# Optimization experiments

Hardware: AMD Instinct MI355X
Metric: run time of the kernel (lower is better)

Reference implementation:

```python
import jax, jax.numpy as jnp
import numpy as np

EPS = 1e-8


def setup_inputs() -> dict:
    key = jax.random.key(0)
    x = jax.random.normal(key, (16384, 1024), dtype=jnp.float32)
    return {"x": x}


def reference(x) -> jnp.ndarray:
    # L2 normalize along feature dim (torch F.normalize: x / max(||x||, eps))
    norm = jnp.linalg.norm(x, axis=-1, keepdims=True)
    xn = x / jnp.maximum(norm, EPS)

    n = xn.shape[0]
    # full pairwise cosine similarity [N, N]
    dot = xn @ xn.T
    # mask self-similarity on the diagonal
    ii = jnp.arange(n)
    dot = dot.at[ii, ii].set(-1.0)
    # nearest neighbor per row
    index = jnp.argmax(dot, axis=1)

    # torch PairwiseDistance(p=2, eps=1e-8): ||x1 - x2 + eps||_2
    diff = xn - xn[index] + EPS
    distances = jnp.linalg.norm(diff, axis=-1)

    loss = -jnp.mean(jnp.log(distances + EPS))
    return loss
```

## Files before the change

kernel.cpp:

```cpp
#include <hip/hip_runtime.h>
#include <math.h>

#define N 16384
#define D 1024
#define EPSF 1e-8f
#define QSCALE 448.0f
#define NPAIRS 2080
#define NBLK 256
#define PANB 262144
#define BIAS 16777216u

typedef __attribute__((ext_vector_type(4))) int i32x4;
typedef unsigned int u32;
typedef unsigned long long u64;

#define LDS_Bb 65536
#define LDS_TOT 131072

__device__ __forceinline__ void gload_lds16(const void* g, void* l) {
  __builtin_amdgcn_global_load_lds(
      (const __attribute__((address_space(1))) u32*)g,
      (__attribute__((address_space(3))) u32*)l, 16, 0, 0);
}

__device__ __forceinline__ u64 maxu64(u64 x, u64 y) { return x > y ? x : y; }
__device__ __forceinline__ int maxi(int x, int y) { return x > y ? x : y; }

__device__ __forceinline__ void decode_pair(int t, int& a, int& b) {
  int aa = (int)((129.0 - sqrt(129.0 * 129.0 - 8.0 * (double)t)) * 0.5);
  if (aa < 0) aa = 0;
  if (aa > 63) aa = 63;
  while (((aa + 1) * 64 - ((aa + 1) * aa) / 2) <= t) ++aa;
  while ((aa * 64 - (aa * (aa - 1)) / 2) > t) --aa;
  a = aa;
  b = aa + (t - (aa * 64 - (aa * (aa - 1)) / 2));
}


__global__ __launch_bounds__(256) void k_normalize(
    const float* __restrict__ x, signed char* __restrict__ xq,
    float* __restrict__ norms, u64* __restrict__ best) {
  const int w = threadIdx.x >> 6, lane = threadIdx.x & 63;
  const int i = blockIdx.x * 4 + w;
  if (threadIdx.x < 4) best[(size_t)blockIdx.x * 4 + threadIdx.x] = 0;
  const float4* xi = (const float4*)(x + (size_t)i * D);
  float4 v[4];
  float s = 0.f;
#pragma unroll
  for (int t = 0; t < 4; ++t) {
    v[t] = xi[lane + t * 64];
    s += v[t].x * v[t].x + v[t].y * v[t].y + v[t].z * v[t].z + v[t].w * v[t].w;
  }
#pragma unroll
  for (int sh = 32; sh; sh >>= 1) s += __shfl_xor(s, sh, 64);
  const float nrm = sqrtf(s);
  if (lane == 0) norms[i] = nrm;
  const float qs = QSCALE / fmaxf(nrm, EPSF);
  u32* xo = (u32*)(xq + (size_t)i * D);
#pragma unroll
  for (int t = 0; t < 4; ++t) {
    const int q0 = __float2int_rn(fminf(fmaxf(v[t].x * qs, -127.f), 127.f));
    const int q1 = __float2int_rn(fminf(fmaxf(v[t].y * qs, -127.f), 127.f));
    const int q2 = __float2int_rn(fminf(fmaxf(v[t].z * qs, -127.f), 127.f));
    const int q3 = __float2int_rn(fminf(fmaxf(v[t].w * qs, -127.f), 127.f));
    xo[lane + t * 64] = (u32)(q0 & 0xff) | ((u32)(q1 & 0xff) << 8) |
                        ((u32)(q2 & 0xff) << 16) | ((u32)(q3 & 0xff) << 24);
  }
}


#define SGB(gaddr, daddr) \
  gload_lds16(xqB + (gaddr) + srcLane, lds + (daddr) + w * 1024)

#define KT(C_)                                                                 \
  {                                                                            \
    const int k_ = kq * 4 + (C_);                                              \
    const int t_ = k_ + 3;                                                     \
    const int kt_ = t_ & 15;                                                   \
    const size_t aG = (t_ >= 16 ? aPanN : aPan) + (size_t)(kt_ * 64);          \
    const size_t bG = (t_ >= 16 ? bPanN : bPan) + (size_t)(kt_ * 64);          \
    __builtin_amdgcn_s_barrier();                                              \
    asm volatile("" ::: "memory");                                             \
    SGB(aG, (((C_) + 3) & 3) * 16384);                                         \
    SGB(aG + 131072, (((C_) + 3) & 3) * 16384 + 8192);                         \
    SGB(bG, LDS_Bb + (((C_) + 3) & 3) * 16384);                                \
    SGB(bG + 131072, LDS_Bb + (((C_) + 3) & 3) * 16384 + 8192);                \
    i32x4 aa[4], bb[4];                                                        \
    _Pragma("unroll") for (int m = 0; m < 4; ++m) aa[m] =                      \
        *(const i32x4*)(lds + ((C_)&3) * 16384 + aOff[m]);                     \
    _Pragma("unroll") for (int n = 0; n < 4; ++n) bb[n] =                      \
        *(const i32x4*)(lds + LDS_Bb + ((C_)&3) * 16384 + bOff[n]);            \
    __builtin_amdgcn_s_setprio(1);                                             \
    _Pragma("unroll") for (int m = 0; m < 4; ++m)                              \
      _Pragma("unroll") for (int n = 0; n < 4; ++n)                            \
        acc[m][n] = __builtin_amdgcn_mfma_i32_16x16x64_i8(aa[m], bb[n],        \
                                                          acc[m][n], 0, 0, 0); \
    __builtin_amdgcn_s_setprio(0);                                             \
    _Pragma("unroll") for (int n = 0; n < 4; ++n) bb[n] =                      \
        *(const i32x4*)(lds + LDS_Bb + ((C_)&3) * 16384 + bOff[4 + n]);        \
    __builtin_amdgcn_s_setprio(1);                                             \
    _Pragma("unroll") for (int m = 0; m < 4; ++m)                              \
      _Pragma("unroll") for (int n = 0; n < 4; ++n)                            \
        acc[m][4 + n] = __builtin_amdgcn_mfma_i32_16x16x64_i8(                 \
            aa[m], bb[n], acc[m][4 + n], 0, 0, 0);                             \
    __builtin_amdgcn_s_setprio(0);                                             \
    asm volatile("s_waitcnt vmcnt(8)" ::: "memory");                           \
  }

__global__ __launch_bounds__(512, 2) void k_argmax(
    const signed char* __restrict__ xq, u64* __restrict__ best) {
  extern __shared__ char lds[];
  const char* xqB = (const char*)xq;
  const int tid = (int)threadIdx.x, lane = tid & 63, w = tid >> 6;
  const int wr = w >> 1, wc = w & 1;

  int aOff[4], bOff[8];
  const int q = lane >> 4, li = lane & 15;
#pragma unroll
  for (int m = 0; m < 4; ++m) {
    const int rr = wr * 64 + m * 16 + li;
    const int line = rr >> 1;
    aOff[m] = line * 128 + ((((rr & 1) << 6) | (q << 4)) ^ ((line & 7) << 4));
  }
#pragma unroll
  for (int nf = 0; nf < 8; ++nf) {
    const int rr = wc * 128 + nf * 16 + li;
    const int line = rr >> 1;
    bOff[nf] = line * 128 + ((((rr & 1) << 6) | (q << 4)) ^ ((line & 7) << 4));
  }
  const int posx = (lane & 7) ^ (lane >> 3);
  const int rrl = ((w * 8 + (lane >> 3)) << 1) | (posx >> 2);
  const int srcLane = rrl * 1024 + (posx & 3) * 16;

  const int rB2 = wr * 64 + (q << 2);
  const int cB2 = wc * 128 + li;

  const int p0 = ((int)blockIdx.x * NPAIRS) / NBLK;
  const int p1 = (((int)blockIdx.x + 1) * NPAIRS) / NBLK;
  int a, b;
  decode_pair(p0, a, b);
  size_t aPan = (size_t)a * PANB, bPan = (size_t)b * PANB;

  for (int pp = 0; pp < 3; ++pp) {
    SGB(aPan + (size_t)(pp * 64), pp * 16384);
    SGB(aPan + (size_t)(pp * 64) + 131072, pp * 16384 + 8192);
    SGB(bPan + (size_t)(pp * 64), LDS_Bb + pp * 16384);
    SGB(bPan + (size_t)(pp * 64) + 131072, LDS_Bb + pp * 16384 + 8192);
  }
  asm volatile("s_waitcnt vmcnt(8)" ::: "memory");

  i32x4 acc[4][8];
  for (int p = p0; p < p1; ++p) {
    int an = a, bn = b + 1;
    if (bn == 64) {
      an = a + 1;
      bn = an;
    }
    const bool lastp = (p == p1 - 1);
    const size_t aPanN = lastp ? aPan : (size_t)an * PANB;
    const size_t bPanN = lastp ? bPan : (size_t)bn * PANB;

#pragma unroll
    for (int m = 0; m < 4; ++m)
#pragma unroll
      for (int n = 0; n < 8; ++n) acc[m][n] = (i32x4){0, 0, 0, 0};

    for (int kq = 0; kq < 4; ++kq) {
      KT(0)
      KT(1)
      KT(2)
      KT(3)
    }

    const int aBase = a * 256, colBase = b * 256;
#pragma unroll
    for (int m = 0; m < 4; ++m)
#pragma unroll
      for (int r = 0; r < 4; ++r) {
        const int rl = rB2 + m * 16 + r;
        int pk = 0;
        if (a == b) {
#pragma unroll
          for (int nf = 0; nf < 8; ++nf) {
            int v = (int)((((u32)acc[m][nf][r] + BIAS) << 7) |
                          (u32)((nf << 4) | li));
            if (rl == cB2 + nf * 16) v = 0;
            pk = maxi(pk, v);
          }
        } else {
#pragma unroll
          for (int nf = 0; nf < 8; ++nf) {
            const int v = (int)((((u32)acc[m][nf][r] + BIAS) << 7) |
                                (u32)((nf << 4) | li));
            pk = maxi(pk, v);
          }
        }
#pragma unroll
        for (int sh = 1; sh < 16; sh <<= 1) pk = maxi(pk, __shfl_xor(pk, sh, 64));
        if (li == 0) {
          const int dot = (int)((((u32)pk) >> 7) - BIAS);
          const int col = colBase + wc * 128 + (pk & 127);
          const u64 key = ((u64)((u32)dot ^ 0x80000000u) << 32) | (u32)col;
          atomicMax(best + (aBase + rl), key);
        }
      }

    if (a != b) {
#pragma unroll
      for (int nf = 0; nf < 8; ++nf) {
        int pk = 0;
#pragma unroll
        for (int m = 0; m < 4; ++m)
#pragma unroll
          for (int r = 0; r < 4; ++r) {
            const int v = (int)((((u32)acc[m][nf][r] + BIAS) << 6) |
                                (u32)(m * 16 + q * 4 + r));
            pk = maxi(pk, v);
          }
        pk = maxi(pk, __shfl_xor(pk, 16, 64));
        pk = maxi(pk, __shfl_xor(pk, 32, 64));
        if (q == 0) {
          const int dot = (int)((((u32)pk) >> 6) - BIAS);
          const int grow = aBase + wr * 64 + (pk & 63);
          const u64 key = ((u64)((u32)dot ^ 0x80000000u) << 32) | (u32)grow;
          atomicMax(best + (colBase + cB2 + nf * 16), key);
        }
      }
    }

    a = an;
    b = bn;
    aPan = (size_t)a * PANB;
    bPan = (size_t)b * PANB;
  }
}


__global__ __launch_bounds__(256) void k_dist(
    const float* __restrict__ x, const float* __restrict__ norms,
    const u64* __restrict__ best, float* __restrict__ logd) {
  const int w = threadIdx.x >> 6, lane = threadIdx.x & 63;
  const int i = blockIdx.x * 4 + w;
  const u64 p = best[i];
  const int j = (int)(p & 0xffffffffu);
  const float invi = 1.f / fmaxf(norms[i], EPSF);
  const float invj = 1.f / fmaxf(norms[j], EPSF);
  const float4* xi = (const float4*)(x + (size_t)i * D);
  const float4* xj = (const float4*)(x + (size_t)j * D);
  float s = 0.f;
#pragma unroll
  for (int t = 0; t < 4; ++t) {
    const float4 av = xi[lane + t * 64], bv = xj[lane + t * 64];
    float d;
    d = av.x * invi - bv.x * invj + EPSF; s += d * d;
    d = av.y * invi - bv.y * invj + EPSF; s += d * d;
    d = av.z * invi - bv.z * invj + EPSF; s += d * d;
    d = av.w * invi - bv.w * invj + EPSF; s += d * d;
  }
#pragma unroll
  for (int sh = 32; sh; sh >>= 1) s += __shfl_xor(s, sh, 64);
  if (lane == 0) logd[i] = logf(sqrtf(s) + EPSF);
}


__global__ __launch_bounds__(256) void k_final(const float* __restrict__ logd,
                                               float* __restrict__ out) {
  __shared__ double red[256];
  double s = 0.0;
  for (int i = threadIdx.x; i < N; i += 256) s += (double)logd[i];
  red[threadIdx.x] = s;
  __syncthreads();
  for (int sh = 128; sh; sh >>= 1) {
    if ((int)threadIdx.x < sh) red[threadIdx.x] += red[threadIdx.x + sh];
    __syncthreads();
  }
  if (threadIdx.x == 0) out[0] = (float)(-red[0] / (double)N);
}


extern "C" void kernel_launch(void* const* d_in, const int* in_sizes, int n_in,
                              void* d_out, int out_size, void* d_ws,
                              size_t ws_size, hipStream_t stream) {
  const float* x = (const float*)d_in[0];
  float* out = (float*)d_out;
  char* ws = (char*)d_ws;

  signed char* xq = (signed char*)ws;
  float* norms = (float*)(ws + 16777216);
  u64* best = (u64*)(ws + 16842752);
  float* logd = (float*)(ws + 16973824);

  k_normalize<<<N / 4, 256, 0, stream>>>(x, xq, norms, best);
  k_argmax<<<NBLK, 512, LDS_TOT, stream>>>(xq, best);
  k_dist<<<N / 4, 256, 0, stream>>>(x, norms, best, logd);
  k_final<<<1, 256, 0, stream>>>(logd, out);
}
```

Measured before the change: 217.3 us.

## Restructure int8 GEMM LDS pipeline into two-tile groups with one barrier each

Replaces the 4-slot ring, which had a prefetch distance of three tiles and a barrier before every k-tile, with groups of two tiles. Each group issues the loads for the next pair of slots, computes the current pair, then waits with vmcnt(0). This halves the number of workgroup barriers, but the full wait on every global-to-LDS load shrinks the latency-hiding window and can stall on memory. The packed argmax keys are also switched from signed to unsigned max, so keys whose bias-shifted value sets the top bit are ordered correctly.

```diff
diff --git a/kernel.cpp b/kernel.cpp
--- a/kernel.cpp
+++ b/kernel.cpp
@@ -23,8 +23,8 @@
       (__attribute__((address_space(3))) u32*)l, 16, 0, 0);
 }
 
-__device__ __forceinline__ u64 maxu64(u64 x, u64 y) { return x > y ? x : y; }
 __device__ __forceinline__ int maxi(int x, int y) { return x > y ? x : y; }
+__device__ __forceinline__ u32 maxu(u32 x, u32 y) { return x > y ? x : y; }
 
 __device__ __forceinline__ void decode_pair(int t, int& a, int& b) {
   int aa = (int)((129.0 - sqrt(129.0 * 129.0 - 8.0 * (double)t)) * 0.5);
@@ -72,24 +72,25 @@
 #define SGB(gaddr, daddr) \
   gload_lds16(xqB + (gaddr) + srcLane, lds + (daddr) + w * 1024)
 
-#define KT(C_)                                                                 \
+#define STAGE2(T_, SLOT_)                                                \
+  {                                                                      \
+    const int t_ = (T_);                                                 \
+    const int kt_ = t_ & 15;                                             \
+    const size_t aG = (t_ >= 16 ? aPanN : aPan) + (size_t)(kt_ * 64);    \
+    const size_t bG = (t_ >= 16 ? bPanN : bPan) + (size_t)(kt_ * 64);    \
+    SGB(aG, (SLOT_)*16384);                                              \
+    SGB(aG + 131072, (SLOT_)*16384 + 8192);                              \
+    SGB(bG, LDS_Bb + (SLOT_)*16384);                                     \
+    SGB(bG + 131072, LDS_Bb + (SLOT_)*16384 + 8192);                     \
+  }
+
+#define CTILE(SLOT_)                                                           \
   {                                                                            \
-    const int k_ = kq * 4 + (C_);                                              \
-    const int t_ = k_ + 3;                                                     \
-    const int kt_ = t_ & 15;                                                   \
-    const size_t aG = (t_ >= 16 ? aPanN : aPan) + (size_t)(kt_ * 64);          \
-    const size_t bG = (t_ >= 16 ? bPanN : bPan) + (size_t)(kt_ * 64);          \
-    __builtin_amdgcn_s_barrier();                                              \
-    asm volatile("" ::: "memory");                                             \
-    SGB(aG, (((C_) + 3) & 3) * 16384);                                         \
-    SGB(aG + 131072, (((C_) + 3) & 3) * 16384 + 8192);                         \
-    SGB(bG, LDS_Bb + (((C_) + 3) & 3) * 16384);                                \
-    SGB(bG + 131072, LDS_Bb + (((C_) + 3) & 3) * 16384 + 8192);                \
     i32x4 aa[4], bb[4];                                                        \
     _Pragma("unroll") for (int m = 0; m < 4; ++m) aa[m] =                      \
-        *(const i32x4*)(lds + ((C_)&3) * 16384 + aOff[m]);                     \
+        *(const i32x4*)(lds + (SLOT_)*16384 + aOff[m]);                        \
     _Pragma("unroll") for (int n = 0; n < 4; ++n) bb[n] =                      \
-        *(const i32x4*)(lds + LDS_Bb + ((C_)&3) * 16384 + bOff[n]);            \
+        *(const i32x4*)(lds + LDS_Bb + (SLOT_)*16384 + bOff[n]);               \
     __builtin_amdgcn_s_setprio(1);                                             \
     _Pragma("unroll") for (int m = 0; m < 4; ++m)                              \
       _Pragma("unroll") for (int n = 0; n < 4; ++n)                            \
@@ -97,14 +98,24 @@
                                                           acc[m][n], 0, 0, 0); \
     __builtin_amdgcn_s_setprio(0);                                             \
     _Pragma("unroll") for (int n = 0; n < 4; ++n) bb[n] =                      \
-        *(const i32x4*)(lds + LDS_Bb + ((C_)&3) * 16384 + bOff[4 + n]);        \
+        *(const i32x4*)(lds + LDS_Bb + (SLOT_)*16384 + bOff[4 + n]);           \
     __builtin_amdgcn_s_setprio(1);                                             \
     _Pragma("unroll") for (int m = 0; m < 4; ++m)                              \
       _Pragma("unroll") for (int n = 0; n < 4; ++n)                            \
         acc[m][4 + n] = __builtin_amdgcn_mfma_i32_16x16x64_i8(                 \
             aa[m], bb[n], acc[m][4 + n], 0, 0, 0);                             \
     __builtin_amdgcn_s_setprio(0);                                             \
-    asm volatile("s_waitcnt vmcnt(8)" ::: "memory");                           \
+  }
+
+#define GROUP(G_)                                                        \
+  {                                                                      \
+    __builtin_amdgcn_s_barrier();                                        \
+    asm volatile("" ::: "memory");                                       \
+    STAGE2(kq * 4 + 2 * (G_) + 2, 2 * ((G_) ^ 1));                       \
+    STAGE2(kq * 4 + 2 * (G_) + 3, 2 * ((G_) ^ 1) + 1);                   \
+    CTILE(2 * (G_));                                                     \
+    CTILE(2 * (G_) + 1);                                                 \
+    asm volatile("s_waitcnt vmcnt(0)" ::: "memory");                     \
   }
 
 __global__ __launch_bounds__(512, 2) void k_argmax(
@@ -140,14 +151,11 @@
   int a, b;
   decode_pair(p0, a, b);
   size_t aPan = (size_t)a * PANB, bPan = (size_t)b * PANB;
-
-  for (int pp = 0; pp < 3; ++pp) {
-    SGB(aPan + (size_t)(pp * 64), pp * 16384);
-    SGB(aPan + (size_t)(pp * 64) + 131072, pp * 16384 + 8192);
-    SGB(bPan + (size_t)(pp * 64), LDS_Bb + pp * 16384);
-    SGB(bPan + (size_t)(pp * 64) + 131072, LDS_Bb + pp * 16384 + 8192);
-  }
-  asm volatile("s_waitcnt vmcnt(8)" ::: "memory");
+  size_t aPanN = aPan, bPanN = bPan;
+
+  STAGE2(0, 0)
+  STAGE2(1, 1)
+  asm volatile("s_waitcnt vmcnt(0)" ::: "memory");
 
   i32x4 acc[4][8];
   for (int p = p0; p < p1; ++p) {
@@ -157,8 +165,8 @@
       bn = an;
     }
     const bool lastp = (p == p1 - 1);
-    const size_t aPanN = lastp ? aPan : (size_t)an * PANB;
-    const size_t bPanN = lastp ? bPan : (size_t)bn * PANB;
+    aPanN = lastp ? aPan : (size_t)an * PANB;
+    bPanN = lastp ? bPan : (size_t)bn * PANB;
 
 #pragma unroll
     for (int m = 0; m < 4; ++m)
@@ -166,10 +174,8 @@
       for (int n = 0; n < 8; ++n) acc[m][n] = (i32x4){0, 0, 0, 0};
 
     for (int kq = 0; kq < 4; ++kq) {
-      KT(0)
-      KT(1)
-      KT(2)
-      KT(3)
+      GROUP(0)
+      GROUP(1)
     }
 
     const int aBase = a * 256, colBase = b * 256;
@@ -178,28 +184,28 @@
 #pragma unroll
       for (int r = 0; r < 4; ++r) {
         const int rl = rB2 + m * 16 + r;
-        int pk = 0;
+        u32 pk = 0;
         if (a == b) {
 #pragma unroll
           for (int nf = 0; nf < 8; ++nf) {
-            int v = (int)((((u32)acc[m][nf][r] + BIAS) << 7) |
-                          (u32)((nf << 4) | li));
+            u32 v = (((u32)acc[m][nf][r] + BIAS) << 7) | (u32)((nf << 4) | li);
             if (rl == cB2 + nf * 16) v = 0;
-            pk = maxi(pk, v);
+            pk = maxu(pk, v);
           }
         } else {
 #pragma unroll
           for (int nf = 0; nf < 8; ++nf) {
-            const int v = (int)((((u32)acc[m][nf][r] + BIAS) << 7) |
-                                (u32)((nf << 4) | li));
-            pk = maxi(pk, v);
+            const u32 v =
+                (((u32)acc[m][nf][r] + BIAS) << 7) | (u32)((nf << 4) | li);
+            pk = maxu(pk, v);
           }
         }
 #pragma unroll
-        for (int sh = 1; sh < 16; sh <<= 1) pk = maxi(pk, __shfl_xor(pk, sh, 64));
+        for (int sh = 1; sh < 16; sh <<= 1)
+          pk = maxu(pk, (u32)__shfl_xor((int)pk, sh, 64));
         if (li == 0) {
-          const int dot = (int)((((u32)pk) >> 7) - BIAS);
-          const int col = colBase + wc * 128 + (pk & 127);
+          const int dot = (int)(pk >> 7) - (int)BIAS;
+          const int col = colBase + wc * 128 + (int)(pk & 127u);
           const u64 key = ((u64)((u32)dot ^ 0x80000000u) << 32) | (u32)col;
           atomicMax(best + (aBase + rl), key);
         }
```

Result: slower. 222.9 us (+2.6%).

## Split each k-tile into four phases interleaving LDS loads with MFMA groups

Applied to the files above, without the earlier changes.

Each k-tile step is broken into four phases. Each phase reads only two B fragments, issues one of the four async global-to-LDS copies, synchronises with a barrier and lgkmcnt wait, then runs 8 MFMAs. The A fragments are read once per tile and kept in registers across phases. The goal is to spread memory traffic more evenly between matrix-core bursts and to reduce register pressure from holding B fragments. The cost is extra barriers per tile: two per phase instead of one per tile. Separately, the packed argmax keys now use unsigned comparisons, because the biased, shifted dot values can exceed the signed int range.

```diff
diff --git a/kernel.cpp b/kernel.cpp
--- a/kernel.cpp
+++ b/kernel.cpp
@@ -23,8 +23,8 @@
       (__attribute__((address_space(3))) u32*)l, 16, 0, 0);
 }
 
-__device__ __forceinline__ u64 maxu64(u64 x, u64 y) { return x > y ? x : y; }
 __device__ __forceinline__ int maxi(int x, int y) { return x > y ? x : y; }
+__device__ __forceinline__ u32 maxu(u32 x, u32 y) { return x > y ? x : y; }
 
 __device__ __forceinline__ void decode_pair(int t, int& a, int& b) {
   int aa = (int)((129.0 - sqrt(129.0 * 129.0 - 8.0 * (double)t)) * 0.5);
@@ -72,39 +72,44 @@
 #define SGB(gaddr, daddr) \
   gload_lds16(xqB + (gaddr) + srcLane, lds + (daddr) + w * 1024)
 
-#define KT(C_)                                                                 \
-  {                                                                            \
-    const int k_ = kq * 4 + (C_);                                              \
-    const int t_ = k_ + 3;                                                     \
-    const int kt_ = t_ & 15;                                                   \
-    const size_t aG = (t_ >= 16 ? aPanN : aPan) + (size_t)(kt_ * 64);          \
-    const size_t bG = (t_ >= 16 ? bPanN : bPan) + (size_t)(kt_ * 64);          \
-    __builtin_amdgcn_s_barrier();                                              \
-    asm volatile("" ::: "memory");                                             \
-    SGB(aG, (((C_) + 3) & 3) * 16384);                                         \
-    SGB(aG + 131072, (((C_) + 3) & 3) * 16384 + 8192);                         \
-    SGB(bG, LDS_Bb + (((C_) + 3) & 3) * 16384);                                \
-    SGB(bG + 131072, LDS_Bb + (((C_) + 3) & 3) * 16384 + 8192);                \
-    i32x4 aa[4], bb[4];                                                        \
-    _Pragma("unroll") for (int m = 0; m < 4; ++m) aa[m] =                      \
-        *(const i32x4*)(lds + ((C_)&3) * 16384 + aOff[m]);                     \
-    _Pragma("unroll") for (int n = 0; n < 4; ++n) bb[n] =                      \
-        *(const i32x4*)(lds + LDS_Bb + ((C_)&3) * 16384 + bOff[n]);            \
-    __builtin_amdgcn_s_setprio(1);                                             \
-    _Pragma("unroll") for (int m = 0; m < 4; ++m)                              \
-      _Pragma("unroll") for (int n = 0; n < 4; ++n)                            \
-        acc[m][n] = __builtin_amdgcn_mfma_i32_16x16x64_i8(aa[m], bb[n],        \
-                                                          acc[m][n], 0, 0, 0); \
-    __builtin_amdgcn_s_setprio(0);                                             \
-    _Pragma("unroll") for (int n = 0; n < 4; ++n) bb[n] =                      \
-        *(const i32x4*)(lds + LDS_Bb + ((C_)&3) * 16384 + bOff[4 + n]);        \
-    __builtin_amdgcn_s_setprio(1);                                             \
-    _Pragma("unroll") for (int m = 0; m < 4; ++m)                              \
-      _Pragma("unroll") for (int n = 0; n < 4; ++n)                            \
-        acc[m][4 + n] = __builtin_amdgcn_mfma_i32_16x16x64_i8(                 \
-            aa[m], bb[n], acc[m][4 + n], 0, 0, 0);                             \
-    __builtin_amdgcn_s_setprio(0);                                             \
-    asm volatile("s_waitcnt vmcnt(8)" ::: "memory");                           \
+#define PH(C_, NLO, RDAA, SG_, VM_)                                           \
+  {                                                                           \
+    if (RDAA) {                                                               \
+      _Pragma("unroll") for (int m = 0; m < 4; ++m) aa[m] =                   \
+          *(const i32x4*)(lds + ((C_)&3) * 16384 + aOff[m]);                  \
+    }                                                                         \
+    i32x4 b0 = *(const i32x4*)(lds + LDS_Bb + ((C_)&3) * 16384 + bOff[NLO]);  \
+    i32x4 b1 =                                                                \
+        *(const i32x4*)(lds + LDS_Bb + ((C_)&3) * 16384 + bOff[(NLO) + 1]);   \
+    SG_;                                                                      \
+    __builtin_amdgcn_s_barrier();                                             \
+    asm volatile("s_waitcnt lgkmcnt(0)" ::: "memory");                        \
+    __builtin_amdgcn_s_setprio(1);                                            \
+    _Pragma("unroll") for (int m = 0; m < 4; ++m) {                           \
+      acc[m][NLO] = __builtin_amdgcn_mfma_i32_16x16x64_i8(aa[m], b0,          \
+                                                          acc[m][NLO], 0, 0,  \
+                                                          0);                 \
+      acc[m][(NLO) + 1] = __builtin_amdgcn_mfma_i32_16x16x64_i8(              \
+          aa[m], b1, acc[m][(NLO) + 1], 0, 0, 0);                             \
+    }                                                                         \
+    __builtin_amdgcn_s_setprio(0);                                            \
+    if (VM_) asm volatile("s_waitcnt vmcnt(8)" ::: "memory");                 \
+    __builtin_amdgcn_s_barrier();                                             \
+    asm volatile("" ::: "memory");                                            \
+  }
+
+#define KT(C_)                                                                \
+  {                                                                           \
+    const int k_ = kq * 4 + (C_);                                             \
+    const int t_ = k_ + 3;                                                    \
+    const int kt_ = t_ & 15;                                                  \
+    const size_t aG = (t_ >= 16 ? aPanN : aPan) + (size_t)(kt_ * 64);         \
+    const size_t bG = (t_ >= 16 ? bPanN : bPan) + (size_t)(kt_ * 64);         \
+    const int sd_ = (((C_) + 3) & 3) * 16384;                                 \
+    PH(C_, 0, 1, SGB(aG, sd_), 0)                                             \
+    PH(C_, 2, 0, SGB(aG + 131072, sd_ + 8192), 0)                             \
+    PH(C_, 4, 0, SGB(bG, LDS_Bb + sd_), 0)                                    \
+    PH(C_, 6, 0, SGB(bG + 131072, LDS_Bb + sd_ + 8192), 1)                    \
   }
 
 __global__ __launch_bounds__(512, 2) void k_argmax(
@@ -148,7 +153,10 @@
     SGB(bPan + (size_t)(pp * 64) + 131072, LDS_Bb + pp * 16384 + 8192);
   }
   asm volatile("s_waitcnt vmcnt(8)" ::: "memory");
-
+  __builtin_amdgcn_s_barrier();
+  asm volatile("" ::: "memory");
+
+  i32x4 aa[4];
   i32x4 acc[4][8];
   for (int p = p0; p < p1; ++p) {
     int an = a, bn = b + 1;
@@ -178,28 +186,28 @@
 #pragma unroll
       for (int r = 0; r < 4; ++r) {
         const int rl = rB2 + m * 16 + r;
-        int pk = 0;
+        u32 pk = 0;
         if (a == b) {
 #pragma unroll
           for (int nf = 0; nf < 8; ++nf) {
-            int v = (int)((((u32)acc[m][nf][r] + BIAS) << 7) |
-                          (u32)((nf << 4) | li));
+            u32 v = (((u32)acc[m][nf][r] + BIAS) << 7) | (u32)((nf << 4) | li);
             if (rl == cB2 + nf * 16) v = 0;
-            pk = maxi(pk, v);
+            pk = maxu(pk, v);
           }
         } else {
 #pragma unroll
           for (int nf = 0; nf < 8; ++nf) {
-            const int v = (int)((((u32)acc[m][nf][r] + BIAS) << 7) |
-                                (u32)((nf << 4) | li));
-            pk = maxi(pk, v);
+            const u32 v =
+                (((u32)acc[m][nf][r] + BIAS) << 7) | (u32)((nf << 4) | li);
+            pk = maxu(pk, v);
           }
         }
 #pragma unroll
-        for (int sh = 1; sh < 16; sh <<= 1) pk = maxi(pk, __shfl_xor(pk, sh, 64));
+        for (int sh = 1; sh < 16; sh <<= 1)
+          pk = maxu(pk, (u32)__shfl_xor((int)pk, sh, 64));
         if (li == 0) {
-          const int dot = (int)((((u32)pk) >> 7) - BIAS);
-          const int col = colBase + wc * 128 + (pk & 127);
+          const int dot = (int)(pk >> 7) - (int)BIAS;
+          const int col = colBase + wc * 128 + (int)(pk & 127u);
           const u64 key = ((u64)((u32)dot ^ 0x80000000u) << 32) | (u32)col;
           atomicMax(best + (aBase + rl), key);
         }
```

Result: slower. 226.1 us (+4.1%).

## Schedule argmax tile pairs dynamically via an atomic work counter

Applied to the files above, without the earlier changes.

Replaces the static split of the 2080 triangular tile pairs across 256 blocks with a global atomic counter that hands out pairs. Each block prefetches the ticket for its next pair one iteration ahead, so the panel prefetch can keep going. The counter is reset in the normalize kernel and the ticket is kept in a small extra LDS slot. This aims to balance uneven per-pair cost, since diagonal tiles skip the column reduction. In exchange it adds per-tile atomics, and it may lose the panel locality of consecutive pairs.

```diff
diff --git a/kernel.cpp b/kernel.cpp
--- a/kernel.cpp
+++ b/kernel.cpp
@@ -15,7 +15,7 @@
 typedef unsigned long long u64;
 
 #define LDS_Bb 65536
-#define LDS_TOT 131072
+#define LDS_TOT 131088
 
 __device__ __forceinline__ void gload_lds16(const void* g, void* l) {
   __builtin_amdgcn_global_load_lds(
@@ -23,8 +23,8 @@
       (__attribute__((address_space(3))) u32*)l, 16, 0, 0);
 }
 
-__device__ __forceinline__ u64 maxu64(u64 x, u64 y) { return x > y ? x : y; }
 __device__ __forceinline__ int maxi(int x, int y) { return x > y ? x : y; }
+__device__ __forceinline__ u32 maxu(u32 x, u32 y) { return x > y ? x : y; }
 
 __device__ __forceinline__ void decode_pair(int t, int& a, int& b) {
   int aa = (int)((129.0 - sqrt(129.0 * 129.0 - 8.0 * (double)t)) * 0.5);
@@ -39,10 +39,11 @@
 
 __global__ __launch_bounds__(256) void k_normalize(
     const float* __restrict__ x, signed char* __restrict__ xq,
-    float* __restrict__ norms, u64* __restrict__ best) {
+    float* __restrict__ norms, u64* __restrict__ best, int* __restrict__ ctr) {
   const int w = threadIdx.x >> 6, lane = threadIdx.x & 63;
   const int i = blockIdx.x * 4 + w;
   if (threadIdx.x < 4) best[(size_t)blockIdx.x * 4 + threadIdx.x] = 0;
+  if (blockIdx.x == 0 && threadIdx.x == 0) *ctr = 0;
   const float4* xi = (const float4*)(x + (size_t)i * D);
   float4 v[4];
   float s = 0.f;
@@ -108,8 +109,10 @@
   }
 
 __global__ __launch_bounds__(512, 2) void k_argmax(
-    const signed char* __restrict__ xq, u64* __restrict__ best) {
+    const signed char* __restrict__ xq, u64* __restrict__ best,
+    int* __restrict__ ctr) {
   extern __shared__ char lds[];
+  int* s_next = (int*)(lds + 131072);
   const char* xqB = (const char*)xq;
   const int tid = (int)threadIdx.x, lane = tid & 63, w = tid >> 6;
   const int wr = w >> 1, wc = w & 1;
@@ -135,10 +138,17 @@
   const int rB2 = wr * 64 + (q << 2);
   const int cB2 = wc * 128 + li;
 
-  const int p0 = ((int)blockIdx.x * NPAIRS) / NBLK;
-  const int p1 = (((int)blockIdx.x + 1) * NPAIRS) / NBLK;
+  if (tid == 0) {
+    s_next[0] = atomicAdd(ctr, 1);
+    s_next[1] = atomicAdd(ctr, 1);
+  }
+  __syncthreads();
+  int pcur = s_next[0], pnext = s_next[1];
+  __syncthreads();
+  if (pcur >= NPAIRS) return;
+
   int a, b;
-  decode_pair(p0, a, b);
+  decode_pair(pcur, a, b);
   size_t aPan = (size_t)a * PANB, bPan = (size_t)b * PANB;
 
   for (int pp = 0; pp < 3; ++pp) {
@@ -149,16 +159,14 @@
   }
   asm volatile("s_waitcnt vmcnt(8)" ::: "memory");
 
+  int par = 0;
   i32x4 acc[4][8];
-  for (int p = p0; p < p1; ++p) {
-    int an = a, bn = b + 1;
-    if (bn == 64) {
-      an = a + 1;
-      bn = an;
-    }
-    const bool lastp = (p == p1 - 1);
-    const size_t aPanN = lastp ? aPan : (size_t)an * PANB;
-    const size_t bPanN = lastp ? bPan : (size_t)bn * PANB;
+  while (true) {
+    const bool hasNext = (pnext < NPAIRS);
+    int an = a, bn = b;
+    if (hasNext) decode_pair(pnext, an, bn);
+    const size_t aPanN = (size_t)an * PANB, bPanN = (size_t)bn * PANB;
+    if (tid == 0) s_next[par] = atomicAdd(ctr, 1);
 
 #pragma unroll
     for (int m = 0; m < 4; ++m)
@@ -178,28 +186,28 @@
 #pragma unroll
       for (int r = 0; r < 4; ++r) {
         const int rl = rB2 + m * 16 + r;
-        int pk = 0;
+        u32 pk = 0;
         if (a == b) {
 #pragma unroll
           for (int nf = 0; nf < 8; ++nf) {
-            int v = (int)((((u32)acc[m][nf][r] + BIAS) << 7) |
-                          (u32)((nf << 4) | li));
+            u32 v = (((u32)acc[m][nf][r] + BIAS) << 7) | (u32)((nf << 4) | li);
             if (rl == cB2 + nf * 16) v = 0;
-            pk = maxi(pk, v);
+            pk = maxu(pk, v);
           }
         } else {
 #pragma unroll
           for (int nf = 0; nf < 8; ++nf) {
-            const int v = (int)((((u32)acc[m][nf][r] + BIAS) << 7) |
-                                (u32)((nf << 4) | li));
-            pk = maxi(pk, v);
+            const u32 v =
+                (((u32)acc[m][nf][r] + BIAS) << 7) | (u32)((nf << 4) | li);
+            pk = maxu(pk, v);
           }
         }
 #pragma unroll
-        for (int sh = 1; sh < 16; sh <<= 1) pk = maxi(pk, __shfl_xor(pk, sh, 64));
+        for (int sh = 1; sh < 16; sh <<= 1)
+          pk = maxu(pk, (u32)__shfl_xor((int)pk, sh, 64));
         if (li == 0) {
-          const int dot = (int)((((u32)pk) >> 7) - BIAS);
-          const int col = colBase + wc * 128 + (pk & 127);
+          const int dot = (int)(pk >> 7) - (int)BIAS;
+          const int col = colBase + wc * 128 + (int)(pk & 127u);
           const u64 key = ((u64)((u32)dot ^ 0x80000000u) << 32) | (u32)col;
           atomicMax(best + (aBase + rl), key);
         }
@@ -228,10 +236,15 @@
       }
     }
 
+    if (!hasNext) break;
+    const int pnn = s_next[par];
+    pcur = pnext;
     a = an;
     b = bn;
-    aPan = (size_t)a * PANB;
-    bPan = (size_t)b * PANB;
+    aPan = aPanN;
+    bPan = bPanN;
+    pnext = pnn;
+    par ^= 1;
   }
 }
 
@@ -289,9 +302,10 @@
   float* norms = (float*)(ws + 16777216);
   u64* best = (u64*)(ws + 16842752);
   float* logd = (float*)(ws + 16973824);
-
-  k_normalize<<<N / 4, 256, 0, stream>>>(x, xq, norms, best);
-  k_argmax<<<NBLK, 512, LDS_TOT, stream>>>(xq, best);
+  int* ctr = (int*)(ws + 17039360);
+
+  k_normalize<<<N / 4, 256, 0, stream>>>(x, xq, norms, best, ctr);
+  k_argmax<<<NBLK, 512, LDS_TOT, stream>>>(xq, best, ctr);
   k_dist<<<N / 4, 256, 0, stream>>>(x, norms, best, logd);
   k_final<<<1, 256, 0, stream>>>(logd, out);
 }
```

After: 233.6 us. 1.08x slower.
